# Optimization experiments

Hardware: AMD Instinct MI355X
Metric: run time of the kernel (lower is better)

Reference implementation:

```python
import jax, jax.numpy as jnp
import numpy as np

CHF_STEP = 32
CHF_TIK = 0.05
SAMPLE_STEP = 1.0
IS_DENSE = False


def _make_templates(H, W, dtype):
    # sample coordinates of pixel centers; x over width (last dim), y over height
    x_axis = SAMPLE_STEP / 2 + SAMPLE_STEP * jnp.arange(W, dtype=dtype)  # (W,)
    y_axis = SAMPLE_STEP / 2 + SAMPLE_STEP * jnp.arange(H, dtype=dtype)  # (H,)
    # matches torch: repeat_interleave(x, H) and y.repeat(W) -> column-major flatten order
    coords = jnp.stack([jnp.repeat(x_axis, H), jnp.tile(y_axis, W)], axis=0)  # (2, N=W*H)
    freq = jnp.arange(-CHF_STEP, CHF_STEP, dtype=dtype) * CHF_TIK  # (2S,)
    S2 = 2 * CHF_STEP
    # plane[u, v] = (freq[v], freq[u])
    plane = jnp.stack([jnp.broadcast_to(freq[None, :], (S2, S2)),
                       jnp.broadcast_to(freq[:, None], (S2, S2))], axis=2)  # (2S, 2S, 2)
    angle = jnp.einsum('uvc,cn->uvn', plane, coords)  # (2S, 2S, N)
    return jnp.cos(angle), jnp.sin(angle)


def setup_inputs() -> dict:
    key = jax.random.key(0)
    k1, k2 = jax.random.split(key)
    B, H, W = 16, 128, 128
    dnn_output = jax.random.uniform(k1, (B, H, W), dtype=jnp.float32)
    chf = jax.random.normal(k2, (B, 2 * CHF_STEP, 2 * CHF_STEP, 2), dtype=jnp.float32)
    return {"dnn_output": dnn_output, "chf": chf}


def reference(dnn_output, chf):
    B, H, W = dnn_output.shape
    real_t, img_t = _make_templates(H, W, dnn_output.dtype)  # (2S,2S,N) each
    # transpose(-1,-2) then flatten -> column-major order matching coords
    flat = jnp.swapaxes(dnn_output, -1, -2).reshape(B, -1)  # (B, N)
    # broadcast-multiply + sum == batched GEMM
    chf_real = jnp.einsum('uvn,bn->buv', real_t, flat)
    chf_img = jnp.einsum('uvn,bn->buv', img_t, flat)
    derived = jnp.stack([chf_real, chf_img], axis=3).astype(chf.dtype)  # (B,2S,2S,2)
    diff = derived - chf
    if IS_DENSE:
        loss = jnp.sum(jnp.linalg.norm(diff, axis=2)) * (CHF_TIK ** 2)
    else:
        loss = jnp.sum(jnp.linalg.norm(diff.reshape(B, -1), axis=1) * CHF_TIK)
    return loss / B
```

## Files before the change

kernel.cpp:

```cpp
#include <hip/hip_runtime.h>
#include <math.h>

#define S2 64
#define HH 128
#define WW 128
#define BB 16
#define TIK 0.05f
#define NG 17
#define NBLK (BB * NG)

#define ROT(c, s, cr, sr)                           \
    {                                               \
        const float _cn = fmaf(c, cr, -(s) * (sr)); \
        s = fmaf(s, cr, (c) * (sr));                \
        c = _cn;                                    \
    }

#define FMA4(acc, sc, v)                \
    acc.x = fmaf(sc, v.x, acc.x);       \
    acc.y = fmaf(sc, v.y, acc.y);       \
    acc.z = fmaf(sc, v.z, acc.z);       \
    acc.w = fmaf(sc, v.w, acc.w);

__global__ __launch_bounds__(256) void chf_main(const float* __restrict__ dnn,
                                                const float* __restrict__ chf,
                                                float* __restrict__ partials) {
    const int bid = blockIdx.x;
    const int b = bid / NG;
    const int g = bid - b * NG;
    const int t = threadIdx.x;
    const bool dual = (g < 16);
    const int uu0 = dual ? (g << 1) : 32;
    const int uu1 = (g << 1) + 1;

    __shared__ float a2r0[8 * WW], a2i0[8 * WW], a2r1[8 * WW], a2i1[8 * WW];
    __shared__ float crw0[WW], ciw0[WW], crw1[WW], ciw1[WW];
    __shared__ float prc0[256], prs0[256], pic0[256], pis0[256];
    __shared__ float prc1[256], prs1[256], pic1[256], pis1[256];

    const float fu0 = (float)(uu0 - 32) * TIK;
    const float fu1 = (float)(uu1 - 32) * TIK;

    float2 cf0 = make_float2(0.f, 0.f), cfm0 = make_float2(0.f, 0.f);
    float2 cf1 = make_float2(0.f, 0.f), cfm1 = make_float2(0.f, 0.f);
    if (t < 64) {
        cf0 = *(const float2*)(chf + ((((size_t)b * S2 + uu0) * S2 + t) * 2));
        if (uu0 >= 1 && uu0 <= 31)
            cfm0 = *(const float2*)(chf + ((((size_t)b * S2 + (64 - uu0)) * S2 + t) * 2));
        if (dual) {
            cf1 = *(const float2*)(chf + ((((size_t)b * S2 + uu1) * S2 + t) * 2));
            cfm1 = *(const float2*)(chf + ((((size_t)b * S2 + (64 - uu1)) * S2 + t) * 2));
        }
    }

    {
        const int hg = t >> 5;
        const int w4 = t & 31;
        const float4* drow = (const float4*)(dnn + (size_t)b * HH * WW);

        const float base = (float)(hg * 16) + 0.5f;
        float c00 = __cosf(fu0 * base), s00 = __sinf(fu0 * base);
        const float cA = __cosf(fu0), sA = __sinf(fu0);
        float c01 = c00, s01 = s00;
        ROT(c01, s01, cA, sA);
        const float c2A = fmaf(cA, cA, -sA * sA), s2A = 2.0f * sA * cA;

        float c10 = 0.f, s10 = 0.f, c11 = 0.f, s11 = 0.f;
        float c2B = 1.f, s2B = 0.f;
        if (dual) {
            c10 = __cosf(fu1 * base); s10 = __sinf(fu1 * base);
            const float cB = __cosf(fu1), sB = __sinf(fu1);
            c11 = c10; s11 = s10;
            ROT(c11, s11, cB, sB);
            c2B = fmaf(cB, cB, -sB * sB); s2B = 2.0f * sB * cB;
        }

        float4 ar0 = {0, 0, 0, 0}, ai0 = {0, 0, 0, 0};
        float4 ar1 = {0, 0, 0, 0}, ai1 = {0, 0, 0, 0};
#pragma unroll
        for (int j = 0; j < 8; ++j) {
            const int h = hg * 16 + 2 * j;
            const float4 d0 = drow[h * (WW / 4) + w4];
            const float4 d1 = drow[(h + 1) * (WW / 4) + w4];
            FMA4(ar0, c00, d0); FMA4(ai0, s00, d0);
            FMA4(ar0, c01, d1); FMA4(ai0, s01, d1);
            FMA4(ar1, c10, d0); FMA4(ai1, s10, d0);
            FMA4(ar1, c11, d1); FMA4(ai1, s11, d1);
            ROT(c00, s00, c2A, s2A);
            ROT(c01, s01, c2A, s2A);
            ROT(c10, s10, c2B, s2B);
            ROT(c11, s11, c2B, s2B);
        }
        const int idx = hg * WW + w4 * 4;
        *(float4*)&a2r0[idx] = ar0;
        *(float4*)&a2i0[idx] = ai0;
        *(float4*)&a2r1[idx] = ar1;
        *(float4*)&a2i1[idx] = ai1;
    }
    __syncthreads();

    if (t < WW) {
        float sr0 = 0, si0 = 0, sr1 = 0, si1 = 0;
#pragma unroll
        for (int k = 0; k < 8; ++k) {
            sr0 += a2r0[k * WW + t];
            si0 += a2i0[k * WW + t];
            sr1 += a2r1[k * WW + t];
            si1 += a2i1[k * WW + t];
        }
        crw0[t] = sr0; ciw0[t] = si0;
        crw1[t] = sr1; ciw1[t] = si1;
    }
    __syncthreads();

    {
        const int v = t & 63;
        const int q = t >> 6;
        const int w0 = q * 32;
        const float fv = (float)(v - 32) * TIK;

        const float a0 = fv * ((float)w0 + 0.5f);
        float c0 = __cosf(a0), s0 = __sinf(a0);
        const float cfv = __cosf(fv), sfv = __sinf(fv);
        float c1 = c0, s1 = s0; ROT(c1, s1, cfv, sfv);
        float c2 = c1, s2 = s1; ROT(c2, s2, cfv, sfv);
        float c3 = c2, s3 = s2; ROT(c3, s3, cfv, sfv);
        const float c2f = fmaf(cfv, cfv, -sfv * sfv);
        const float s2f = 2.0f * sfv * cfv;
        const float c4f = fmaf(c2f, c2f, -s2f * s2f);
        const float s4f = 2.0f * s2f * c2f;

        float rc0 = 0, rs0 = 0, ic0 = 0, is0 = 0;
        float rc1 = 0, rs1 = 0, ic1 = 0, is1 = 0;
#define BSTEP(CK, SK, W)                                          \
        {                                                         \
            const float cr0v = crw0[W], ci0v = ciw0[W];           \
            const float cr1v = crw1[W], ci1v = ciw1[W];           \
            rc0 = fmaf(CK, cr0v, rc0); rs0 = fmaf(SK, cr0v, rs0); \
            ic0 = fmaf(CK, ci0v, ic0); is0 = fmaf(SK, ci0v, is0); \
            rc1 = fmaf(CK, cr1v, rc1); rs1 = fmaf(SK, cr1v, rs1); \
            ic1 = fmaf(CK, ci1v, ic1); is1 = fmaf(SK, ci1v, is1); \
        }
#pragma unroll
        for (int j = 0; j < 8; ++j) {
            const int w = w0 + 4 * j;
            BSTEP(c0, s0, w);
            BSTEP(c1, s1, w + 1);
            BSTEP(c2, s2, w + 2);
            BSTEP(c3, s3, w + 3);
            ROT(c0, s0, c4f, s4f);
            ROT(c1, s1, c4f, s4f);
            ROT(c2, s2, c4f, s4f);
            ROT(c3, s3, c4f, s4f);
        }
#undef BSTEP
        prc0[t] = rc0; prs0[t] = rs0; pic0[t] = ic0; pis0[t] = is0;
        prc1[t] = rc1; prs1[t] = rs1; pic1[t] = ic1; pis1[t] = is1;
    }
    __syncthreads();

    if (t < 64) {
        const float rc = prc0[t] + prc0[t + 64] + prc0[t + 128] + prc0[t + 192];
        const float rs = prs0[t] + prs0[t + 64] + prs0[t + 128] + prs0[t + 192];
        const float ic = pic0[t] + pic0[t + 64] + pic0[t + 128] + pic0[t + 192];
        const float is_ = pis0[t] + pis0[t + 64] + pis0[t + 128] + pis0[t + 192];

        const float d0 = (rc - is_) - cf0.x;
        const float d1 = (rs + ic) - cf0.y;
        float sq = fmaf(d0, d0, d1 * d1);
        if (uu0 >= 1 && uu0 <= 31) {
            const float d2 = (rc + is_) - cfm0.x;
            const float d3 = (rs - ic) - cfm0.y;
            sq = fmaf(d2, d2, sq);
            sq = fmaf(d3, d3, sq);
        }

        if (dual) {
            const float rcB = prc1[t] + prc1[t + 64] + prc1[t + 128] + prc1[t + 192];
            const float rsB = prs1[t] + prs1[t + 64] + prs1[t + 128] + prs1[t + 192];
            const float icB = pic1[t] + pic1[t + 64] + pic1[t + 128] + pic1[t + 192];
            const float isB = pis1[t] + pis1[t + 64] + pis1[t + 128] + pis1[t + 192];

            const float e0 = (rcB - isB) - cf1.x;
            const float e1 = (rsB + icB) - cf1.y;
            sq = fmaf(e0, e0, sq);
            sq = fmaf(e1, e1, sq);
            const float e2 = (rcB + isB) - cfm1.x;
            const float e3 = (rsB - icB) - cfm1.y;
            sq = fmaf(e2, e2, sq);
            sq = fmaf(e3, e3, sq);
        }
#pragma unroll
        for (int off = 32; off; off >>= 1)
            sq += __shfl_down(sq, off, 64);
        if (t == 0) partials[bid] = sq;
    }
}

__global__ __launch_bounds__(512) void chf_final(const float* __restrict__ partials,
                                                 float* __restrict__ out) {
    const int t = threadIdx.x;
    const int b = t >> 5;
    const int l = t & 31;
    __shared__ float red[BB];
    float v = (l < NG) ? partials[b * NG + l] : 0.0f;
#pragma unroll
    for (int off = 16; off; off >>= 1)
        v += __shfl_down(v, off, 32);
    if (l == 0) red[b] = sqrtf(v);
    __syncthreads();
    if (t == 0) {
        float acc = 0;
#pragma unroll
        for (int i = 0; i < BB; ++i) acc += red[i];
        out[0] = acc * (TIK / (float)BB);
    }
}

extern "C" void kernel_launch(void* const* d_in, const int* in_sizes, int n_in,
                              void* d_out, int out_size, void* d_ws, size_t ws_size,
                              hipStream_t stream) {
    const float* dnn = (const float*)d_in[0];
    const float* chf = (const float*)d_in[1];
    float* out = (float*)d_out;
    float* partials = (float*)d_ws;

    chf_main<<<dim3(NBLK), dim3(256), 0, stream>>>(dnn, chf, partials);
    chf_final<<<dim3(1), dim3(512), 0, stream>>>(partials, out);
}
```

Measured before the change: 11.75 us.

## Fuse final reduction into main kernel via flag-based inter-block handoff

Removes the second kernel launch by having the 17th block of each batch spin on global magic-value flags to gather the 16 partials, compute the per-batch norm, and pass it to the last batch's block for the final sum. Flags are consumed with an atomic exchange that resets them, so they can be reused across calls without clearing the workspace. This saves a launch and its gap but depends on all producer blocks being co-resident or scheduled before the spinning consumers (272 blocks fits the device), and it relies on the workspace flags never accidentally holding the magic values.

New measurement: 16.21 us. 1.38x slower.

```diff
diff --git a/kernel.cpp b/kernel.cpp
--- a/kernel.cpp
+++ b/kernel.cpp
@@ -8,6 +8,8 @@
 #define TIK 0.05f
 #define NG 17
 #define NBLK (BB * NG)
+#define MAGIC1 0x5EEDF00Du
+#define MAGIC2 0xC0FFEE42u
 
 #define ROT(c, s, cr, sr)                           \
     {                                               \
@@ -22,9 +24,21 @@
     acc.z = fmaf(sc, v.z, acc.z);       \
     acc.w = fmaf(sc, v.w, acc.w);
 
-__global__ __launch_bounds__(256) void chf_main(const float* __restrict__ dnn,
-                                                const float* __restrict__ chf,
-                                                float* __restrict__ partials) {
+__device__ __forceinline__ void consume_flag(unsigned int* f, unsigned int magic) {
+    while (__hip_atomic_exchange(f, 0u, __ATOMIC_ACQUIRE,
+                                 __HIP_MEMORY_SCOPE_AGENT) != magic)
+        __builtin_amdgcn_s_sleep(1);
+}
+
+__global__ __launch_bounds__(256) void chf_fused(const float* __restrict__ dnn,
+                                                 const float* __restrict__ chf,
+                                                 float* __restrict__ part,
+                                                 unsigned int* __restrict__ pf1,
+                                                 unsigned int* __restrict__ pf2,
+                                                 float* __restrict__ bres,
+                                                 unsigned int* __restrict__ bf1,
+                                                 unsigned int* __restrict__ bf2,
+                                                 float* __restrict__ out) {
     const int bid = blockIdx.x;
     const int b = bid / NG;
     const int g = bid - b * NG;
@@ -37,6 +51,8 @@
     __shared__ float crw0[WW], ciw0[WW], crw1[WW], ciw1[WW];
     __shared__ float prc0[256], prs0[256], pic0[256], pis0[256];
     __shared__ float prc1[256], prs1[256], pic1[256], pis1[256];
+    __shared__ float gather[16];
+    __shared__ float batch_r[BB - 1];
 
     const float fu0 = (float)(uu0 - 32) * TIK;
     const float fu1 = (float)(uu1 - 32) * TIK;
@@ -159,6 +175,7 @@
     }
     __syncthreads();
 
+    float sq = 0.0f;
     if (t < 64) {
         const float rc = prc0[t] + prc0[t + 64] + prc0[t + 128] + prc0[t + 192];
         const float rs = prs0[t] + prs0[t + 64] + prs0[t + 128] + prs0[t + 192];
@@ -167,7 +184,7 @@
 
         const float d0 = (rc - is_) - cf0.x;
         const float d1 = (rs + ic) - cf0.y;
-        float sq = fmaf(d0, d0, d1 * d1);
+        sq = fmaf(d0, d0, d1 * d1);
         if (uu0 >= 1 && uu0 <= 31) {
             const float d2 = (rc + is_) - cfm0.x;
             const float d3 = (rs - ic) - cfm0.y;
@@ -193,27 +210,53 @@
 #pragma unroll
         for (int off = 32; off; off >>= 1)
             sq += __shfl_down(sq, off, 64);
-        if (t == 0) partials[bid] = sq;
-    }
-}
-
-__global__ __launch_bounds__(512) void chf_final(const float* __restrict__ partials,
-                                                 float* __restrict__ out) {
-    const int t = threadIdx.x;
-    const int b = t >> 5;
-    const int l = t & 31;
-    __shared__ float red[BB];
-    float v = (l < NG) ? partials[b * NG + l] : 0.0f;
-#pragma unroll
-    for (int off = 16; off; off >>= 1)
-        v += __shfl_down(v, off, 32);
-    if (l == 0) red[b] = sqrtf(v);
+    }
+
+    if (dual) {
+        if (t == 0) {
+            const int slot = b * 16 + g;
+            __hip_atomic_store(&part[slot], sq, __ATOMIC_RELAXED, __HIP_MEMORY_SCOPE_AGENT);
+            __hip_atomic_store(&pf1[slot], MAGIC1, __ATOMIC_RELEASE, __HIP_MEMORY_SCOPE_AGENT);
+            __hip_atomic_store(&pf2[slot], MAGIC2, __ATOMIC_RELEASE, __HIP_MEMORY_SCOPE_AGENT);
+        }
+        return;
+    }
+
+    if (t < 16) {
+        const int slot = b * 16 + t;
+        consume_flag(&pf1[slot], MAGIC1);
+        consume_flag(&pf2[slot], MAGIC2);
+        gather[t] = __hip_atomic_load(&part[slot], __ATOMIC_RELAXED, __HIP_MEMORY_SCOPE_AGENT);
+    }
+    __syncthreads();
+
+    if (b < BB - 1) {
+        if (t == 0) {
+            float acc = sq;
+#pragma unroll
+            for (int i = 0; i < 16; ++i) acc += gather[i];
+            const float r = sqrtf(acc);
+            __hip_atomic_store(&bres[b], r, __ATOMIC_RELAXED, __HIP_MEMORY_SCOPE_AGENT);
+            __hip_atomic_store(&bf1[b], MAGIC1, __ATOMIC_RELEASE, __HIP_MEMORY_SCOPE_AGENT);
+            __hip_atomic_store(&bf2[b], MAGIC2, __ATOMIC_RELEASE, __HIP_MEMORY_SCOPE_AGENT);
+        }
+        return;
+    }
+
+    if (t < BB - 1) {
+        consume_flag(&bf1[t], MAGIC1);
+        consume_flag(&bf2[t], MAGIC2);
+        batch_r[t] = __hip_atomic_load(&bres[t], __ATOMIC_RELAXED, __HIP_MEMORY_SCOPE_AGENT);
+    }
     __syncthreads();
     if (t == 0) {
-        float acc = 0;
-#pragma unroll
-        for (int i = 0; i < BB; ++i) acc += red[i];
-        out[0] = acc * (TIK / (float)BB);
+        float acc = sq;
+#pragma unroll
+        for (int i = 0; i < 16; ++i) acc += gather[i];
+        float tot = sqrtf(acc);
+#pragma unroll
+        for (int i = 0; i < BB - 1; ++i) tot += batch_r[i];
+        out[0] = tot * (TIK / (float)BB);
     }
 }
 
@@ -223,8 +266,14 @@
     const float* dnn = (const float*)d_in[0];
     const float* chf = (const float*)d_in[1];
     float* out = (float*)d_out;
-    float* partials = (float*)d_ws;
-
-    chf_main<<<dim3(NBLK), dim3(256), 0, stream>>>(dnn, chf, partials);
-    chf_final<<<dim3(1), dim3(512), 0, stream>>>(partials, out);
+
+    float* part = (float*)d_ws;
+    unsigned int* pf1 = (unsigned int*)d_ws + 256;
+    unsigned int* pf2 = (unsigned int*)d_ws + 512;
+    float* bres = (float*)d_ws + 768;
+    unsigned int* bf1 = (unsigned int*)d_ws + 784;
+    unsigned int* bf2 = (unsigned int*)d_ws + 800;
+
+    chf_fused<<<dim3(NBLK), dim3(256), 0, stream>>>(dnn, chf, part, pf1, pf2,
+                                                    bres, bf1, bf2, out);
 }
```
